# Optimization experiments

Hardware: AMD Instinct MI355X
Metric: run time of the kernel (lower is better)

## Reference

```python
import jax, jax.numpy as jnp
import numpy as np

COMMITMENT_COST = 0.25
CODE_BOOK_SIZE = 1024
EMBED_DIM = 64


def setup_inputs() -> dict:
    key = jax.random.key(0)
    k1, k2 = jax.random.split(key)
    inputs = jax.random.normal(k1, (32, 64, 32, 32), dtype=jnp.float32)
    # matches torch init: uniform(-1/K, 1/K)
    embedding = jax.random.uniform(
        k2, (CODE_BOOK_SIZE, EMBED_DIM), dtype=jnp.float32,
        minval=-1.0 / CODE_BOOK_SIZE, maxval=1.0 / CODE_BOOK_SIZE)
    return {"inputs": inputs, "embedding": embedding}


def reference(inputs, embedding):
    # inputs: [B, D, H, W] -> [B, H, W, D]
    x = jnp.transpose(inputs, (0, 2, 3, 1))
    B, H, W, D = x.shape
    flat = x.reshape(-1, D)                                   # [N, D]
    # ((x - e)**2).mean(-1), without the [N, K, D] broadcast tensor)
    x2 = jnp.sum(flat * flat, axis=1, keepdims=True)          # [N, 1]
    e2 = jnp.sum(embedding * embedding, axis=1)               # [K]
    distances = (x2 - 2.0 * (flat @ embedding.T) + e2) / D    # [N, K]
    encoding_indices = jnp.argmin(distances, axis=1)          # [N]
    quantized = embedding[encoding_indices].reshape(B, H, W, D)
    e_latent_loss = jnp.mean((jax.lax.stop_gradient(quantized) - x) ** 2)
    q_latent_loss = jnp.mean((quantized - jax.lax.stop_gradient(x)) ** 2)
    loss = q_latent_loss + COMMITMENT_COST * e_latent_loss
    # straight-through estimator (training mode); value identical to quantized
    quantized = x + jax.lax.stop_gradient(quantized - x)
    return (loss,
            jnp.transpose(quantized, (0, 3, 1, 2)),
            encoding_indices.reshape(B, -1))
```

## Files before the change

kernel.cpp:

```cpp
#include <hip/hip_runtime.h>


constexpr int D_   = 64;
constexpr int HW   = 1024;
constexpr int K_   = 1024;
constexpr int PTS  = 128;
constexpr int CK   = 512;
constexpr int SEC  = 520;
constexpr int QE   = 2097152;
constexpr int IDX_OFF = 1 + QE;

__global__ __launch_bounds__(1024, 4) void vq_main_kernel(
    const float* __restrict__ in, const float* __restrict__ emb,
    float* __restrict__ out, float* __restrict__ loss_acc,
    unsigned* __restrict__ cnt) {
  __shared__ float eTs[D_ * SEC];
  __shared__ float e2s[K_];
  __shared__ float x2s[PTS];
  __shared__ int   idx_sel[PTS];
  __shared__ float redbuf[8];

  const int t    = threadIdx.x;
  const int lane = t & 63;
  const int wv   = t >> 6;
  const int p0   = wv * 8;
  const int blk  = blockIdx.x;
  const int b    = blk >> 3;
  const int hw0  = (blk & 7) * PTS;
  const float* inb = in + b * (D_ * HW) + hw0;

  const int kl = t & 511;
  const int h2 = t >> 9;
  const int pos = ((kl >> 2) & 1) * 256 + (kl >> 3) * 4 + (kl & 3);

  {
    const float4* e4 = (const float4*)(emb + t * 64);
    float s = 0.f;
#pragma unroll
    for (int q = 0; q < 16; ++q) {
      float4 v = e4[q];
      s += v.x * v.x; s += v.y * v.y; s += v.z * v.z; s += v.w * v.w;
    }
    e2s[t] = s;
  }

  {
    const float4* g = (const float4*)(emb + kl * 64 + h2 * 32);
    float4 pf[8];
#pragma unroll
    for (int r = 0; r < 8; ++r) pf[r] = g[r];
#pragma unroll
    for (int r = 0; r < 8; ++r) {
      int d = h2 * 32 + r * 4;
      eTs[(d + 0) * SEC + pos] = pf[r].x;
      eTs[(d + 1) * SEC + pos] = pf[r].y;
      eTs[(d + 2) * SEC + pos] = pf[r].z;
      eTs[(d + 3) * SEC + pos] = pf[r].w;
    }
  }

  if (t < PTS) {
    float s = 0.f;
#pragma unroll 8
    for (int d = 0; d < D_; ++d) { float xv = inb[d * HW + t]; s = fmaf(xv, xv, s); }
    x2s[t] = s;
  }
  __syncthreads();

  float minv[8]; int mini[8];
#pragma unroll
  for (int i = 0; i < 8; ++i) { minv[i] = 3.4e38f; mini[i] = 0; }

#pragma unroll 1
  for (int c = 0; c < 2; ++c) {
    float acc[8][8];
#pragma unroll
    for (int i = 0; i < 8; ++i)
#pragma unroll
      for (int j = 0; j < 8; ++j) acc[i][j] = 0.f;

    const float* xp = inb + p0;
    const float* ep = &eTs[lane * 4];
#pragma unroll 2
    for (int d = 0; d < D_; ++d) {
      float4 xa = *(const float4*)(xp);
      float4 xb = *(const float4*)(xp + 4);
      float4 e0 = *(const float4*)(ep);
      float4 e1 = *(const float4*)(ep + 256);
      xp += HW; ep += SEC;
      float xf[8] = {xa.x, xa.y, xa.z, xa.w, xb.x, xb.y, xb.z, xb.w};
      float ef[8] = {e0.x, e0.y, e0.z, e0.w, e1.x, e1.y, e1.z, e1.w};
#pragma unroll
      for (int i = 0; i < 8; ++i)
#pragma unroll
        for (int j = 0; j < 8; ++j)
          acc[i][j] = fmaf(xf[i], ef[j], acc[i][j]);
    }

    float x2v[8];
    {
      float4 xa = *(const float4*)&x2s[p0];
      float4 xb = *(const float4*)&x2s[p0 + 4];
      x2v[0]=xa.x; x2v[1]=xa.y; x2v[2]=xa.z; x2v[3]=xa.w;
      x2v[4]=xb.x; x2v[5]=xb.y; x2v[6]=xb.z; x2v[7]=xb.w;
    }
    float e2f[8];
    {
      const float4* p4 = (const float4*)&e2s[c * CK + lane * 8];
      float4 v0 = p4[0], v1 = p4[1];
      e2f[0]=v0.x; e2f[1]=v0.y; e2f[2]=v0.z; e2f[3]=v0.w;
      e2f[4]=v1.x; e2f[5]=v1.y; e2f[6]=v1.z; e2f[7]=v1.w;
    }
#pragma unroll
    for (int j = 0; j < 8; ++j) {
      int cg = c * CK + lane * 8 + j;
      float e2v = e2f[j];
#pragma unroll
      for (int i = 0; i < 8; ++i) {
        float u = fmaf(-2.f, acc[i][j], x2v[i]) + e2v;
        if (u < minv[i]) { minv[i] = u; mini[i] = cg; }
      }
    }

    if (c == 0) {
      __syncthreads();
      const float4* g = (const float4*)(emb + (CK + kl) * 64 + h2 * 32);
      float4 pf[8];
#pragma unroll
      for (int r = 0; r < 8; ++r) pf[r] = g[r];
#pragma unroll
      for (int r = 0; r < 8; ++r) {
        int d = h2 * 32 + r * 4;
        eTs[(d + 0) * SEC + pos] = pf[r].x;
        eTs[(d + 1) * SEC + pos] = pf[r].y;
        eTs[(d + 2) * SEC + pos] = pf[r].z;
        eTs[(d + 3) * SEC + pos] = pf[r].w;
      }
      __syncthreads();
    }
  }

#pragma unroll
  for (int i = 0; i < 8; ++i) {
    float v = minv[i]; int ix = mini[i];
#pragma unroll
    for (int off = 1; off < 64; off <<= 1) {
      float vo = __shfl_xor(v, off);
      int   io = __shfl_xor(ix, off);
      if (vo < v || (vo == v && io < ix)) { v = vo; ix = io; }
    }
    if (lane == 0) idx_sel[p0 + i] = ix;
  }
  __syncthreads();

  if (t < PTS) out[IDX_OFF + blk * PTS + t] = (float)idx_sel[t];

  float* outq = out + 1 + b * (D_ * HW) + hw0;
  float lp = 0.f;
  if (t < 512) {
#pragma unroll
    for (int i = 0; i < 4; ++i) {
      int fi = t + i * 512;
      int p = fi & 127, qd = fi >> 7;
      int cidx = idx_sel[p];
      float4 q = *(const float4*)(emb + cidx * 64 + qd * 4);
      float xv0 = inb[(qd * 4 + 0) * HW + p];
      float xv1 = inb[(qd * 4 + 1) * HW + p];
      float xv2 = inb[(qd * 4 + 2) * HW + p];
      float xv3 = inb[(qd * 4 + 3) * HW + p];
      float d0 = q.x - xv0, d1 = q.y - xv1, d2 = q.z - xv2, d3 = q.w - xv3;
      lp = fmaf(d0, d0, lp); lp = fmaf(d1, d1, lp);
      lp = fmaf(d2, d2, lp); lp = fmaf(d3, d3, lp);
      outq[(qd * 4 + 0) * HW + p] = xv0 + d0;
      outq[(qd * 4 + 1) * HW + p] = xv1 + d1;
      outq[(qd * 4 + 2) * HW + p] = xv2 + d2;
      outq[(qd * 4 + 3) * HW + p] = xv3 + d3;
    }

#pragma unroll
    for (int off = 1; off < 64; off <<= 1) lp += __shfl_xor(lp, off);
    if ((t & 63) == 0) redbuf[t >> 6] = lp;
  }
  __syncthreads();
  if (t == 0) {
    float part = 0.f;
#pragma unroll
    for (int w = 0; w < 8; ++w) part += redbuf[w];
    atomicAdd(loss_acc, part);
    __threadfence();
    unsigned old = atomicAdd(cnt, 1u);
    if (old == 255u) {
      __threadfence();
      float total = atomicAdd(loss_acc, 0.0f);
      float m = total * (1.0f / 2097152.0f);
      out[0] = m + 0.25f * m;
    }
  }
}

extern "C" void kernel_launch(void* const* d_in, const int* in_sizes, int n_in,
                              void* d_out, int out_size, void* d_ws, size_t ws_size,
                              hipStream_t stream) {
  const float* in  = (const float*)d_in[0];
  const float* emb = (const float*)d_in[1];
  float* out = (float*)d_out;
  float* loss_acc = (float*)d_ws;
  unsigned* cnt   = (unsigned*)d_ws + 4;

  hipMemsetAsync(d_ws, 0, 64, stream);
  vq_main_kernel<<<256, 1024, 0, stream>>>(in, emb, out, loss_acc, cnt);
}
```

Measured before the change: 145.8 us.

## Stage inputs in LDS and software-pipeline codebook half-tiles through registers

```diff
diff --git a/kernel.cpp b/kernel.cpp
--- a/kernel.cpp
+++ b/kernel.cpp
@@ -6,7 +6,8 @@
 constexpr int K_   = 1024;
 constexpr int PTS  = 128;
 constexpr int CK   = 512;
-constexpr int SEC  = 520;
+constexpr int DH   = 32;
+constexpr int SP   = 132;
 constexpr int QE   = 2097152;
 constexpr int IDX_OFF = 1 + QE;
 
@@ -14,7 +15,8 @@
     const float* __restrict__ in, const float* __restrict__ emb,
     float* __restrict__ out, float* __restrict__ loss_acc,
     unsigned* __restrict__ cnt) {
-  __shared__ float eTs[D_ * SEC];
+  __shared__ float eTs[DH * CK];
+  __shared__ float xT[D_ * SP];
   __shared__ float e2s[K_];
   __shared__ float x2s[PTS];
   __shared__ int   idx_sel[PTS];
@@ -30,8 +32,15 @@
   const float* inb = in + b * (D_ * HW) + hw0;
 
   const int kl = t & 511;
-  const int h2 = t >> 9;
+  const int h  = t >> 9;
   const int pos = ((kl >> 2) & 1) * 256 + (kl >> 3) * 4 + (kl & 3);
+
+#pragma unroll
+  for (int i = 0; i < 2; ++i) {
+    int fi = t + i * 1024;
+    int d  = fi >> 5, p4 = fi & 31;
+    *(float4*)(&xT[d * SP + p4 * 4]) = *(const float4*)(inb + d * HW + p4 * 4);
+  }
 
   {
     const float4* e4 = (const float4*)(emb + t * 64);
@@ -45,24 +54,25 @@
   }
 
   {
-    const float4* g = (const float4*)(emb + kl * 64 + h2 * 32);
-    float4 pf[8];
-#pragma unroll
-    for (int r = 0; r < 8; ++r) pf[r] = g[r];
-#pragma unroll
-    for (int r = 0; r < 8; ++r) {
-      int d = h2 * 32 + r * 4;
-      eTs[(d + 0) * SEC + pos] = pf[r].x;
-      eTs[(d + 1) * SEC + pos] = pf[r].y;
-      eTs[(d + 2) * SEC + pos] = pf[r].z;
-      eTs[(d + 3) * SEC + pos] = pf[r].w;
-    }
-  }
+    const float4* g = (const float4*)(emb + kl * 64 + h * 16);
+    float4 pf[4];
+#pragma unroll
+    for (int r = 0; r < 4; ++r) pf[r] = g[r];
+#pragma unroll
+    for (int r = 0; r < 4; ++r) {
+      int dq = h * 16 + r * 4;
+      eTs[(dq + 0) * CK + pos] = pf[r].x;
+      eTs[(dq + 1) * CK + pos] = pf[r].y;
+      eTs[(dq + 2) * CK + pos] = pf[r].z;
+      eTs[(dq + 3) * CK + pos] = pf[r].w;
+    }
+  }
+  __syncthreads();
 
   if (t < PTS) {
     float s = 0.f;
 #pragma unroll 8
-    for (int d = 0; d < D_; ++d) { float xv = inb[d * HW + t]; s = fmaf(xv, xv, s); }
+    for (int d = 0; d < D_; ++d) { float xv = xT[d * SP + t]; s = fmaf(xv, xv, s); }
     x2s[t] = s;
   }
   __syncthreads();
@@ -79,22 +89,48 @@
 #pragma unroll
       for (int j = 0; j < 8; ++j) acc[i][j] = 0.f;
 
-    const float* xp = inb + p0;
-    const float* ep = &eTs[lane * 4];
-#pragma unroll 2
-    for (int d = 0; d < D_; ++d) {
-      float4 xa = *(const float4*)(xp);
-      float4 xb = *(const float4*)(xp + 4);
-      float4 e0 = *(const float4*)(ep);
-      float4 e1 = *(const float4*)(ep + 256);
-      xp += HW; ep += SEC;
-      float xf[8] = {xa.x, xa.y, xa.z, xa.w, xb.x, xb.y, xb.z, xb.w};
-      float ef[8] = {e0.x, e0.y, e0.z, e0.w, e1.x, e1.y, e1.z, e1.w};
-#pragma unroll
-      for (int i = 0; i < 8; ++i)
-#pragma unroll
-        for (int j = 0; j < 8; ++j)
-          acc[i][j] = fmaf(xf[i], ef[j], acc[i][j]);
+#pragma unroll 1
+    for (int dh = 0; dh < 2; ++dh) {
+      const int s = c * 2 + dh;
+      float4 pf[4];
+      if (s < 3) {
+        const int cn = (s + 1) >> 1, dn = (s + 1) & 1;
+        const float4* g =
+            (const float4*)(emb + (cn * CK + kl) * 64 + dn * DH + h * 16);
+#pragma unroll
+        for (int r = 0; r < 4; ++r) pf[r] = g[r];
+      }
+
+      const float* ep = &eTs[lane * 4];
+      const float* xp = &xT[dh * DH * SP + p0];
+#pragma unroll 8
+      for (int dd = 0; dd < DH; ++dd) {
+        float4 e0 = *(const float4*)(ep);
+        float4 e1 = *(const float4*)(ep + 256);
+        float4 xa = *(const float4*)(xp);
+        float4 xb = *(const float4*)(xp + 4);
+        ep += CK; xp += SP;
+        float xf[8] = {xa.x, xa.y, xa.z, xa.w, xb.x, xb.y, xb.z, xb.w};
+        float ef[8] = {e0.x, e0.y, e0.z, e0.w, e1.x, e1.y, e1.z, e1.w};
+#pragma unroll
+        for (int i = 0; i < 8; ++i)
+#pragma unroll
+          for (int j = 0; j < 8; ++j)
+            acc[i][j] = fmaf(xf[i], ef[j], acc[i][j]);
+      }
+
+      if (s < 3) {
+        __syncthreads();
+#pragma unroll
+        for (int r = 0; r < 4; ++r) {
+          int dq = h * 16 + r * 4;
+          eTs[(dq + 0) * CK + pos] = pf[r].x;
+          eTs[(dq + 1) * CK + pos] = pf[r].y;
+          eTs[(dq + 2) * CK + pos] = pf[r].z;
+          eTs[(dq + 3) * CK + pos] = pf[r].w;
+        }
+        __syncthreads();
+      }
     }
 
     float x2v[8];
@@ -121,23 +157,6 @@
         if (u < minv[i]) { minv[i] = u; mini[i] = cg; }
       }
     }
-
-    if (c == 0) {
-      __syncthreads();
-      const float4* g = (const float4*)(emb + (CK + kl) * 64 + h2 * 32);
-      float4 pf[8];
-#pragma unroll
-      for (int r = 0; r < 8; ++r) pf[r] = g[r];
-#pragma unroll
-      for (int r = 0; r < 8; ++r) {
-        int d = h2 * 32 + r * 4;
-        eTs[(d + 0) * SEC + pos] = pf[r].x;
-        eTs[(d + 1) * SEC + pos] = pf[r].y;
-        eTs[(d + 2) * SEC + pos] = pf[r].z;
-        eTs[(d + 3) * SEC + pos] = pf[r].w;
-      }
-      __syncthreads();
-    }
   }
 
 #pragma unroll
@@ -164,10 +183,10 @@
       int p = fi & 127, qd = fi >> 7;
       int cidx = idx_sel[p];
       float4 q = *(const float4*)(emb + cidx * 64 + qd * 4);
-      float xv0 = inb[(qd * 4 + 0) * HW + p];
-      float xv1 = inb[(qd * 4 + 1) * HW + p];
-      float xv2 = inb[(qd * 4 + 2) * HW + p];
-      float xv3 = inb[(qd * 4 + 3) * HW + p];
+      float xv0 = xT[(qd * 4 + 0) * SP + p];
+      float xv1 = xT[(qd * 4 + 1) * SP + p];
+      float xv2 = xT[(qd * 4 + 2) * SP + p];
+      float xv3 = xT[(qd * 4 + 3) * SP + p];
       float d0 = q.x - xv0, d1 = q.y - xv1, d2 = q.z - xv2, d3 = q.w - xv3;
       lp = fmaf(d0, d0, lp); lp = fmaf(d1, d1, lp);
       lp = fmaf(d2, d2, lp); lp = fmaf(d3, d3, lp);
```

New measurement: 154.1 us. 5.7% more time.
